# Kernel optimization log

Measured on AMD Instinct MI355X. Metric: run time of the kernel, lower is better.

## Reference

```python
import jax, jax.numpy as jnp
import numpy as np

N_NODES = 10000
N_EDGES = 640000
NF = 64    # node_feature_size
EF = 64    # edge_feature_size
NH = 128   # node_hidden_size
EH = 128   # edge_hidden_size
CS = 128   # context_size


def _linear_init(key, fan_in, shape):
    bound = 1.0 / np.sqrt(fan_in)
    return jax.random.uniform(key, shape, jnp.float32, -bound, bound)


def setup_inputs() -> dict:
    key = jax.random.key(0)
    ks = jax.random.split(key, 20)
    node_feats = jax.random.normal(ks[0], (N_NODES, NF), jnp.float32)
    edge_feats = jax.random.normal(ks[1], (N_EDGES, EF), jnp.float32)
    src = jax.random.randint(ks[2], (N_EDGES,), 0, N_NODES, jnp.int32)
    dst = jax.random.randint(ks[3], (N_EDGES,), 0, N_NODES, jnp.int32)
    return {
        "node_feats": node_feats,
        "edge_feats": edge_feats,
        "W_node": _linear_init(ks[4], NF, (NF, NH)),
        "b_node": _linear_init(ks[5], NF, (NH,)),
        "W_edge": _linear_init(ks[6], NF + EF, (NF + EF, EH)),
        "b_edge": _linear_init(ks[7], NF + EF, (EH,)),
        "W_logit": _linear_init(ks[8], NH + EH, (NH + EH, 1)),
        "b_logit": _linear_init(ks[9], NH + EH, (1,)),
        "W_msg": _linear_init(ks[10], EH, (EH, CS)),
        "b_msg": _linear_init(ks[11], EH, (CS,)),
        "W_ih": _linear_init(ks[12], NH, (3 * NH, CS)),   # torch GRUCell weight_ih layout
        "W_hh": _linear_init(ks[13], NH, (3 * NH, NH)),
        "b_ih": _linear_init(ks[14], NH, (3 * NH,)),
        "b_hh": _linear_init(ks[15], NH, (3 * NH,)),
        "src": src,
        "dst": dst,
    }


def reference(node_feats, edge_feats, W_node, b_node, W_edge, b_edge,
              W_logit, b_logit, W_msg, b_msg, W_ih, W_hh, b_ih, b_hh,
              src, dst):
    n_nodes = node_feats.shape[0]
    # (1) embed nodes: h_v = LeakyReLU(Linear(f_v))
    h_v = jax.nn.leaky_relu(node_feats @ W_node + b_node)          # [N, NH]
    # (2) embed edges from [src node feats, edge feats]
    e_in = jnp.concatenate([node_feats[src], edge_feats], axis=1)  # [M, NF+EF]
    h_e = jax.nn.leaky_relu(e_in @ W_edge + b_edge)                # [M, EH]
    # raw messages T(h_w->v)
    m = h_e @ W_msg + b_msg                                        # [M, CS]
    # (3) attention logits from [src node hidden, edge hidden]
    l_in = jnp.concatenate([h_v[src], h_e], axis=1)                # [M, NH+EH]
    logit = jax.nn.leaky_relu(l_in @ W_logit + b_logit)            # [M, 1]
    # (4) edge softmax grouped by destination node
    lmax = jax.ops.segment_max(logit, dst, num_segments=n_nodes)   # [N, 1]
    ex = jnp.exp(logit - lmax[dst])
    den = jax.ops.segment_sum(ex, dst, num_segments=n_nodes)       # [N, 1]
    alpha = ex / den[dst]                                          # [M, 1]
    # (5) weighted segment-sum context, then elu
    C_v = jax.ops.segment_sum(alpha * m, dst, num_segments=n_nodes)  # [N, CS]
    C_v = jax.nn.elu(C_v)
    # (6) GRUCell(input=C_v, hidden=h_v), torch semantics, then ReLU
    gi = C_v @ W_ih.T + b_ih                                       # [N, 3*NH]
    gh = h_v @ W_hh.T + b_hh
    i_r, i_z, i_n = jnp.split(gi, 3, axis=1)
    h_r, h_z, h_n = jnp.split(gh, 3, axis=1)
    r = jax.nn.sigmoid(i_r + h_r)
    z = jax.nn.sigmoid(i_z + h_z)
    n = jnp.tanh(i_n + r * h_n)
    h_new = jax.nn.relu((1.0 - z) * n + z * h_v)                   # [N, NH]
    # update_edges=False -> return original edge feats alongside new node states
    return h_new, edge_feats
```

## Files before the change

### kernel.cpp

```cpp
#include <hip/hip_runtime.h>
#include <hip/hip_bf16.h>

typedef unsigned short u16;
typedef unsigned int u32;

typedef __attribute__((ext_vector_type(8))) short bf16x8;
typedef __attribute__((ext_vector_type(4))) float f32x4;

__device__ __forceinline__ u16 f2bf(float f) {
    u32 u = __float_as_uint(f);
    u32 r = ((u >> 16) & 1u) + 0x7fffu;
    return (u16)((u + r) >> 16);
}
__device__ __forceinline__ float bf2f(u16 u) {
    return __uint_as_float(((u32)u) << 16);
}
__device__ __forceinline__ float leaky(float x) { return x >= 0.f ? x : 0.01f * x; }

__global__ __launch_bounds__(256) void k_prep_transpose(
    const float* __restrict__ We, u16* __restrict__ WeT)
{
    int idx = blockIdx.x * 256 + threadIdx.x;
    int r = (idx >> 7) & 127;
    int c = idx & 127;
    WeT[c * 128 + r] = f2bf(We[r * 128 + c]);
}

__global__ __launch_bounds__(256) void k_csr_count(
    const int* __restrict__ dst, u32* __restrict__ deg, int nE)
{
    long e = (long)blockIdx.x * 256 + threadIdx.x;
    if (e >= nE) return;
    atomicAdd(&deg[dst[e]], 1u);
}

__global__ __launch_bounds__(256) void k_csr_scan(
    const u32* __restrict__ deg, u32* __restrict__ start,
    u32* __restrict__ cur, int nN)
{
    __shared__ u32 s[256];
    int t = threadIdx.x;
    int chunk = (nN + 255) / 256;
    int a = t * chunk;
    int b = a + chunk; if (b > nN) b = nN; if (a > nN) a = nN;
    u32 sum = 0;
    for (int i = a; i < b; i++) sum += deg[i];
    s[t] = sum;
    __syncthreads();
    for (int d = 1; d < 256; d <<= 1) {
        u32 v = (t >= d) ? s[t - d] : 0u;
        __syncthreads();
        s[t] += v;
        __syncthreads();
    }
    u32 base = (t == 0) ? 0u : s[t - 1];
    for (int i = a; i < b; i++) { start[i] = base; cur[i] = base; base += deg[i]; }
}

__global__ __launch_bounds__(256) void k_csr_scatter(
    const int* __restrict__ src, const int* __restrict__ dst,
    u32* __restrict__ cur, int* __restrict__ sEidG,
    int* __restrict__ sSrcG, int* __restrict__ sDstG,
    int* __restrict__ rank, int nE)
{
    long e = (long)blockIdx.x * 256 + threadIdx.x;
    if (e >= nE) return;
    int d = dst[e];
    u32 p = atomicAdd(&cur[d], 1u);
    sEidG[p] = (int)e;
    sSrcG[p] = src[e];
    sDstG[p] = d;
    rank[e] = (int)p;
}

__global__ __launch_bounds__(128) void k_node_embed(
    const float* __restrict__ nf, const float* __restrict__ Wn,
    const float* __restrict__ bn, const float* __restrict__ WL,
    float* __restrict__ h_v, float* __restrict__ g, int nN)
{
    __shared__ float sW[64][128];
    __shared__ float sF[8][64];
    __shared__ float sRed[2][8];
    int j = threadIdx.x;
    int n0 = blockIdx.x * 8;
    for (int i = 0; i < 64; i++) sW[i][j] = Wn[i * 128 + j];
    for (int t = j; t < 8 * 64; t += 128) {
        int n = t >> 6, k = t & 63;
        int nn = n0 + n; if (nn >= nN) nn = nN - 1;
        sF[n][k] = nf[(long)nn * 64 + k];
    }
    __syncthreads();
    float bj = bn[j];
    float wl = WL[j];
    int wv = j >> 6, ln = j & 63;
    float hval[8];
    for (int n = 0; n < 8; n++) {
        float acc = bj;
        #pragma unroll 16
        for (int k = 0; k < 64; k++) acc += sF[n][k] * sW[k][j];
        float h = leaky(acc);
        hval[n] = h;
        if (n0 + n < nN) h_v[(long)(n0 + n) * 128 + j] = h;
    }
    #pragma unroll
    for (int n = 0; n < 8; n++) {
        float part = hval[n] * wl;
        #pragma unroll
        for (int o = 1; o < 64; o <<= 1) part += __shfl_xor(part, o);
        if (ln == 0) sRed[wv][n] = part;
    }
    __syncthreads();
    if (j < 8 && n0 + j < nN) g[n0 + j] = sRed[0][j] + sRed[1][j];
}

__device__ __forceinline__ void stage_ein(
    u16 (*sIn)[136], const float* nf, const float* ef,
    const int* sSrc, long e0, int nE, int tid)
{
    for (int c = tid; c < 64 * 32; c += 256) {
        int e = c >> 5, p = c & 31;
        long eg = e0 + e; if (eg >= nE) eg = nE - 1;
        float4 v;
        if (p < 16) v = *((const float4*)(nf + (long)sSrc[e] * 64 + p * 4));
        else        v = *((const float4*)(ef + eg * 64 + (p - 16) * 4));
        u32 lo = (u32)f2bf(v.x) | ((u32)f2bf(v.y) << 16);
        u32 hi = (u32)f2bf(v.z) | ((u32)f2bf(v.w) << 16);
        *((u32*)&sIn[e][p * 4])     = lo;
        *((u32*)&sIn[e][p * 4 + 2]) = hi;
    }
}

template<bool WRITE_HE>
__global__ __launch_bounds__(256) void k_edge_logit(
    const float* __restrict__ nf, const float* __restrict__ ef,
    const int* __restrict__ src, const int* __restrict__ rank,
    const u16* __restrict__ WeT, const float* __restrict__ be,
    const float* __restrict__ WL, const float* __restrict__ bL,
    const float* __restrict__ g,
    float* __restrict__ logitS, u16* __restrict__ heG, int nE)
{
    __shared__ u16 sW[128][136];
    __shared__ u16 sIn[64][136];
    __shared__ float sWL2[128];
    __shared__ int sSrc[64];
    __shared__ int sRank[64];
    int tid = threadIdx.x;
    long e0 = (long)blockIdx.x * 64;
    if (tid < 64) {
        long eg = e0 + tid; if (eg >= nE) eg = nE - 1;
        sSrc[tid] = src[eg];
        sRank[tid] = rank[eg];
    } else if (tid < 192) {
        sWL2[tid - 64] = WL[tid + 64];
    }
    __syncthreads();
    for (int c = tid; c < 2048; c += 256) {
        int r = c >> 4, p = c & 15;
        *((uint4*)&sW[r][p * 8]) = *((const uint4*)(WeT + r * 128 + p * 8));
    }
    stage_ein(sIn, nf, ef, sSrc, e0, nE, tid);
    __syncthreads();

    int lane = tid & 63, w = tid >> 6;
    int nl = lane & 15, q = lane >> 4;
    f32x4 acc[8];
    #pragma unroll
    for (int t = 0; t < 8; t++) acc[t] = (f32x4){0.f, 0.f, 0.f, 0.f};
    int eA = w * 16 + nl;
    #pragma unroll
    for (int s = 0; s < 4; s++) {
        int k0 = s * 32 + q * 8;
        bf16x8 a = *((const bf16x8*)&sIn[eA][k0]);
        #pragma unroll
        for (int t = 0; t < 8; t++) {
            bf16x8 b = *((const bf16x8*)&sW[t * 16 + nl][k0]);
            acc[t] = __builtin_amdgcn_mfma_f32_16x16x32_bf16(a, b, acc[t], 0, 0, 0);
        }
    }
    #pragma unroll
    for (int t = 0; t < 8; t++) {
        int col = t * 16 + nl;
        float bias = be[col];
        #pragma unroll
        for (int r = 0; r < 4; r++) {
            int e = w * 16 + q * 4 + r;
            sIn[e][col] = f2bf(leaky(acc[t][r] + bias));
        }
    }
    if (WRITE_HE) {
        #pragma unroll
        for (int i = 0; i < 4; i++) {
            int row = w * 16 + i * 4 + (lane >> 4);
            int ch = lane & 15;
            long eg = e0 + row;
            uint4 v4 = *((const uint4*)&sIn[row][ch * 8]);
            if (eg < nE) *((uint4*)(heG + eg * 128 + ch * 8)) = v4;
        }
    }
    int ew = lane >> 2, sub = lane & 3;
    int e = w * 16 + ew;
    float sum = 0.f;
    #pragma unroll
    for (int i = 0; i < 4; i++) {
        bf16x8 hv = *((const bf16x8*)&sIn[e][sub * 32 + i * 8]);
        #pragma unroll
        for (int jj = 0; jj < 8; jj++)
            sum += bf2f((u16)hv[jj]) * sWL2[sub * 32 + i * 8 + jj];
    }
    sum += __shfl_xor(sum, 1);
    sum += __shfl_xor(sum, 2);
    if (sub == 0 && e0 + e < nE) {
        float l = leaky(sum + g[sSrc[e]] + bL[0]);
        logitS[sRank[e]] = l;
    }
}

__global__ __launch_bounds__(256) void k_softmax_node(
    const u32* __restrict__ start, const u32* __restrict__ deg,
    float* __restrict__ logitS, int nN)
{
    int v = blockIdx.x * 4 + (threadIdx.x >> 6);
    int lane = threadIdx.x & 63;
    if (v >= nN) return;
    u32 d = deg[v];
    if (d == 0) return;
    u32 s0 = start[v];
    float mx = -3.402823e38f;
    for (u32 i = lane; i < d; i += 64) mx = fmaxf(mx, logitS[s0 + i]);
    #pragma unroll
    for (int o = 1; o < 64; o <<= 1) mx = fmaxf(mx, __shfl_xor(mx, o));
    float sum = 0.f;
    for (u32 i = lane; i < d; i += 64) {
        float e = __expf(logitS[s0 + i] - mx);
        logitS[s0 + i] = e;
        sum += e;
    }
    #pragma unroll
    for (int o = 1; o < 64; o <<= 1) sum += __shfl_xor(sum, o);
    float inv = 1.f / sum;
    for (u32 i = lane; i < d; i += 64) logitS[s0 + i] *= inv;
}

__global__ __launch_bounds__(256) void k_msg_lite(
    const u16* __restrict__ heG, const float* __restrict__ alphaS,
    const int* __restrict__ sEidG, const int* __restrict__ sDstG,
    float* __restrict__ A, int nE)
{
    __shared__ float sAl[256];
    __shared__ int sEid[256];
    __shared__ int sDst[256];
    int tid = threadIdx.x;
    long p0 = (long)blockIdx.x * 256;
    long p = p0 + tid;
    if (p < nE) {
        sAl[tid] = alphaS[p];
        sEid[tid] = sEidG[p];
        sDst[tid] = sDstG[p];
    } else {
        sAl[tid] = 0.f;
        sEid[tid] = sEidG[nE - 1];
        sDst[tid] = sDstG[nE - 1];
    }
    __syncthreads();
    int lane = tid & 63, w = tid >> 6;
    int i0 = w * 64;
    float sx = 0.f, sy = 0.f;
    int curd = sDst[i0];
    #pragma unroll 4
    for (int i = 0; i < 64; i++) {
        int idx = i0 + i;
        float a = sAl[idx];
        const u16* row = heG + (long)sEid[idx] * 128;
        sx += a * bf2f(row[lane]);
        sy += a * bf2f(row[lane + 64]);
        int nxt = (i == 63) ? -1 : sDst[idx + 1];
        if (nxt != curd) {
            atomicAdd(&A[(long)curd * 128 + lane], sx);
            atomicAdd(&A[(long)curd * 128 + lane + 64], sy);
            sx = 0.f; sy = 0.f;
            curd = nxt;
        }
    }
}

__global__ __launch_bounds__(256) void k_msg_heavy(
    const float* __restrict__ nf, const float* __restrict__ ef,
    const int* __restrict__ sEidG, const int* __restrict__ sSrcG,
    const int* __restrict__ sDstG,
    const u16* __restrict__ WeT, const float* __restrict__ be,
    const float* __restrict__ alphaS,
    float* __restrict__ A, int nE)
{
    __shared__ u16 sW[128][136];
    __shared__ u16 sIn[64][136];
    __shared__ float sAlpha[64];
    __shared__ int sSrc[64];
    __shared__ int sEid[64];
    __shared__ int sDst[64];
    int tid = threadIdx.x;
    long p0 = (long)blockIdx.x * 64;
    if (tid < 64) {
        long p = p0 + tid;
        if (p < nE) {
            sEid[tid] = sEidG[p];
            sSrc[tid] = sSrcG[p];
            sDst[tid] = sDstG[p];
            sAlpha[tid] = alphaS[p];
        } else {
            sEid[tid] = sEidG[nE - 1];
            sSrc[tid] = sSrcG[nE - 1];
            sDst[tid] = sDstG[nE - 1];
            sAlpha[tid] = 0.f;
        }
    }
    __syncthreads();
    for (int c = tid; c < 2048; c += 256) {
        int r = c >> 4, pp = c & 15;
        *((uint4*)&sW[r][pp * 8]) = *((const uint4*)(WeT + r * 128 + pp * 8));
    }
    for (int c = tid; c < 64 * 32; c += 256) {
        int e = c >> 5, pp = c & 31;
        float4 v;
        if (pp < 16) v = *((const float4*)(nf + (long)sSrc[e] * 64 + pp * 4));
        else         v = *((const float4*)(ef + (long)sEid[e] * 64 + (pp - 16) * 4));
        u32 lo = (u32)f2bf(v.x) | ((u32)f2bf(v.y) << 16);
        u32 hi = (u32)f2bf(v.z) | ((u32)f2bf(v.w) << 16);
        *((u32*)&sIn[e][pp * 4])     = lo;
        *((u32*)&sIn[e][pp * 4 + 2]) = hi;
    }
    __syncthreads();

    int lane = tid & 63, w = tid >> 6;
    int nl = lane & 15, q = lane >> 4;
    f32x4 acc[8];
    #pragma unroll
    for (int t = 0; t < 8; t++) acc[t] = (f32x4){0.f, 0.f, 0.f, 0.f};
    int eA = w * 16 + nl;
    #pragma unroll
    for (int s = 0; s < 4; s++) {
        int k0 = s * 32 + q * 8;
        bf16x8 a = *((const bf16x8*)&sIn[eA][k0]);
        #pragma unroll
        for (int t = 0; t < 8; t++) {
            bf16x8 b = *((const bf16x8*)&sW[t * 16 + nl][k0]);
            acc[t] = __builtin_amdgcn_mfma_f32_16x16x32_bf16(a, b, acc[t], 0, 0, 0);
        }
    }
    #pragma unroll
    for (int t = 0; t < 8; t++) {
        int col = t * 16 + nl;
        float bias = be[col];
        #pragma unroll
        for (int r = 0; r < 4; r++) {
            int e = w * 16 + q * 4 + r;
            sIn[e][col] = f2bf(leaky(acc[t][r] + bias));
        }
    }
    int eb = w * 16;
    float sx = 0.f, sy = 0.f;
    int curd = sDst[eb];
    for (int i = 0; i < 16; i++) {
        int e = eb + i;
        float a = sAlpha[e];
        sx += a * bf2f(sIn[e][lane]);
        sy += a * bf2f(sIn[e][lane + 64]);
        int nxt = (i == 15) ? -1 : sDst[e + 1];
        if (nxt != curd) {
            atomicAdd(&A[(long)curd * 128 + lane], sx);
            atomicAdd(&A[(long)curd * 128 + lane + 64], sy);
            sx = 0.f; sy = 0.f;
            curd = nxt;
        }
    }
}

__global__ __launch_bounds__(128) void k_gru(
    const float* __restrict__ h_v, const float* __restrict__ A,
    const float* __restrict__ Wm, const float* __restrict__ bm,
    const u32* __restrict__ deg,
    const float* __restrict__ Wih, const float* __restrict__ Whh,
    const float* __restrict__ bih, const float* __restrict__ bhh,
    float* __restrict__ out, int nN)
{
    __shared__ float sA[8][128];
    __shared__ float sC[8][128];
    __shared__ float sH[8][128];
    int j = threadIdx.x;
    int n0 = blockIdx.x * 8;
    for (int n = 0; n < 8; n++) {
        int nn = n0 + n; if (nn >= nN) nn = nN - 1;
        sA[n][j] = A[(long)nn * 128 + j];
        sH[n][j] = h_v[(long)nn * 128 + j];
    }
    __syncthreads();
    float cc[8];
    {
        float bmj = bm[j];
        #pragma unroll
        for (int n = 0; n < 8; n++) cc[n] = bmj;
        for (int k = 0; k < 128; k++) {
            float wk = Wm[(long)k * 128 + j];
            #pragma unroll
            for (int n = 0; n < 8; n++) cc[n] += sA[n][k] * wk;
        }
    }
    for (int n = 0; n < 8; n++) {
        int nn = n0 + n; if (nn >= nN) nn = nN - 1;
        float c = cc[n];
        sC[n][j] = (deg[nn] > 0u) ? (c > 0.f ? c : __expf(c) - 1.f) : 0.f;
    }
    __syncthreads();
    float gi[3][8], gh[3][8];
    #pragma unroll
    for (int g = 0; g < 3; g++) {
        float bi = bih[g * 128 + j];
        float bh = bhh[g * 128 + j];
        #pragma unroll
        for (int n = 0; n < 8; n++) { gi[g][n] = bi; gh[g][n] = bh; }
    }
    for (int k = 0; k < 128; k += 4) {
        float4 cv[8], hv[8];
        #pragma unroll
        for (int n = 0; n < 8; n++) {
            cv[n] = *(const float4*)&sC[n][k];
            hv[n] = *(const float4*)&sH[n][k];
        }
        #pragma unroll
        for (int g = 0; g < 3; g++) {
            float4 wi = *((const float4*)(Wih + (long)(g * 128 + j) * 128 + k));
            float4 wh = *((const float4*)(Whh + (long)(g * 128 + j) * 128 + k));
            #pragma unroll
            for (int n = 0; n < 8; n++) {
                gi[g][n] += wi.x * cv[n].x + wi.y * cv[n].y + wi.z * cv[n].z + wi.w * cv[n].w;
                gh[g][n] += wh.x * hv[n].x + wh.y * hv[n].y + wh.z * hv[n].z + wh.w * hv[n].w;
            }
        }
    }
    #pragma unroll
    for (int n = 0; n < 8; n++) {
        if (n0 + n >= nN) break;
        float r = 1.f / (1.f + __expf(-(gi[0][n] + gh[0][n])));
        float z = 1.f / (1.f + __expf(-(gi[1][n] + gh[1][n])));
        float nn = tanhf(gi[2][n] + r * gh[2][n]);
        float h = (1.f - z) * nn + z * sH[n][j];
        out[(long)(n0 + n) * 128 + j] = (h > 0.f ? h : 0.f);
    }
}

extern "C" void kernel_launch(void* const* d_in, const int* in_sizes, int n_in,
                              void* d_out, int out_size, void* d_ws, size_t ws_size,
                              hipStream_t stream) {
    const float* nf  = (const float*)d_in[0];
    const float* ef  = (const float*)d_in[1];
    const float* Wn  = (const float*)d_in[2];
    const float* bn  = (const float*)d_in[3];
    const float* We  = (const float*)d_in[4];
    const float* be  = (const float*)d_in[5];
    const float* WL  = (const float*)d_in[6];
    const float* bL  = (const float*)d_in[7];
    const float* Wm  = (const float*)d_in[8];
    const float* bm  = (const float*)d_in[9];
    const float* Wih = (const float*)d_in[10];
    const float* Whh = (const float*)d_in[11];
    const float* bih = (const float*)d_in[12];
    const float* bhh = (const float*)d_in[13];
    const int* src = (const int*)d_in[14];
    const int* dst = (const int*)d_in[15];
    float* out = (float*)d_out;

    int nN = in_sizes[0] / 64;
    int nE = in_sizes[1] / 64;

    size_t o = 0;
    auto nxt = [&](size_t b) { size_t p = o; o += (b + 255) & ~(size_t)255; return p; };
    size_t o_hv    = nxt((size_t)nN * 128 * 4);
    size_t o_g     = nxt((size_t)nN * 4);
    size_t o_logit = nxt((size_t)nE * 4);
    size_t o_A     = nxt((size_t)nN * 128 * 4);
    size_t o_deg   = nxt((size_t)nN * 4);
    size_t o_start = nxt((size_t)nN * 4);
    size_t o_cur   = nxt((size_t)nN * 4);
    size_t o_eid   = nxt((size_t)nE * 4);
    size_t o_srcS  = nxt((size_t)nE * 4);
    size_t o_dstS  = nxt((size_t)nE * 4);
    size_t o_rank  = nxt((size_t)nE * 4);
    size_t o_WeT   = nxt((size_t)128 * 128 * 2);
    size_t o_he    = nxt((size_t)nE * 128 * 2);
    bool lite = (o <= ws_size);

    char* w = (char*)d_ws;
    float* h_v    = (float*)(w + o_hv);
    float* g      = (float*)(w + o_g);
    float* logitS = (float*)(w + o_logit);
    float* A      = (float*)(w + o_A);
    u32*   deg    = (u32*)(w + o_deg);
    u32*   start  = (u32*)(w + o_start);
    u32*   cur    = (u32*)(w + o_cur);
    int*   sEid   = (int*)(w + o_eid);
    int*   sSrcS  = (int*)(w + o_srcS);
    int*   sDstS  = (int*)(w + o_dstS);
    int*   rank   = (int*)(w + o_rank);
    u16*   WeT    = (u16*)(w + o_WeT);
    u16*   heG    = (u16*)(w + o_he);

    hipMemsetAsync(A, 0, o_start - o_A, stream);

    int gN8   = (nN + 7) / 8;
    int gN4   = (nN + 3) / 4;
    int gE64  = (nE + 63) / 64;
    int gE256 = (nE + 255) / 256;

    k_prep_transpose<<<64, 256, 0, stream>>>(We, WeT);
    k_csr_count<<<gE256, 256, 0, stream>>>(dst, deg, nE);
    k_csr_scan<<<1, 256, 0, stream>>>(deg, start, cur, nN);
    k_csr_scatter<<<gE256, 256, 0, stream>>>(src, dst, cur, sEid, sSrcS, sDstS, rank, nE);
    k_node_embed<<<gN8, 128, 0, stream>>>(nf, Wn, bn, WL, h_v, g, nN);
    if (lite) {
        k_edge_logit<true><<<gE64, 256, 0, stream>>>(
            nf, ef, src, rank, WeT, be, WL, bL, g, logitS, heG, nE);
    } else {
        k_edge_logit<false><<<gE64, 256, 0, stream>>>(
            nf, ef, src, rank, WeT, be, WL, bL, g, logitS, heG, nE);
    }
    k_softmax_node<<<gN4, 256, 0, stream>>>(start, deg, logitS, nN);
    if (lite) {
        k_msg_lite<<<gE256, 256, 0, stream>>>(heG, logitS, sEid, sDstS, A, nE);
    } else {
        k_msg_heavy<<<gE64, 256, 0, stream>>>(nf, ef, sEid, sSrcS, sDstS,
                                              WeT, be, logitS, A, nE);
    }
    k_gru<<<gN8, 128, 0, stream>>>(h_v, A, Wm, bm, deg,
                                   Wih, Whh, bih, bhh, out, nN);

    hipMemcpyAsync(out + (size_t)nN * 128, ef, (size_t)nE * 64 * 4,
                   hipMemcpyDeviceToDevice, stream);
}
```

Before: 829.4 us.

## Process edges in dst-sorted order, fuse softmax with aggregation, drop atomics and memcpy

The edge-logit kernel now walks edges in CSR (destination-sorted) order, so logits and h_e rows land contiguously and the rank array goes away. Edge softmax and the weighted message sum are fused into one per-node wavefront kernel that accumulates h_e rows directly, with no atomics, and writes A once. The edge-feature passthrough copy is folded into the edge kernel's staging loads instead of a separate memcpy. The weight tile is split into two 64-row halves to cut LDS use and raise occupancy. The tradeoff is uncoalesced gathers of edge_feats by sorted eid, a serial per-node loop whose length follows degree, and a memset narrowed to deg only.

```diff
diff --git a/kernel.cpp b/kernel.cpp
--- a/kernel.cpp
+++ b/kernel.cpp
@@ -60,8 +60,7 @@
 __global__ __launch_bounds__(256) void k_csr_scatter(
     const int* __restrict__ src, const int* __restrict__ dst,
     u32* __restrict__ cur, int* __restrict__ sEidG,
-    int* __restrict__ sSrcG, int* __restrict__ sDstG,
-    int* __restrict__ rank, int nE)
+    int* __restrict__ sSrcG, int* __restrict__ sDstG, int nE)
 {
     long e = (long)blockIdx.x * 256 + threadIdx.x;
     if (e >= nE) return;
@@ -70,7 +69,6 @@
     sEidG[p] = (int)e;
     sSrcG[p] = src[e];
     sDstG[p] = d;
-    rank[e] = (int)p;
 }
 
 __global__ __launch_bounds__(128) void k_node_embed(
@@ -113,68 +111,88 @@
     if (j < 8 && n0 + j < nN) g[n0 + j] = sRed[0][j] + sRed[1][j];
 }
 
-__device__ __forceinline__ void stage_ein(
-    u16 (*sIn)[136], const float* nf, const float* ef,
-    const int* sSrc, long e0, int nE, int tid)
-{
-    for (int c = tid; c < 64 * 32; c += 256) {
+template<bool WRITE_HE>
+__global__ __launch_bounds__(256, 4) void k_edge_logit(
+    const float* __restrict__ nf, const float* __restrict__ ef,
+    const int* __restrict__ sEidG, const int* __restrict__ sSrcG,
+    const u16* __restrict__ WeT, const float* __restrict__ be,
+    const float* __restrict__ WL, const float* __restrict__ bL,
+    const float* __restrict__ g,
+    float* __restrict__ logitS, u16* __restrict__ heG,
+    float* __restrict__ efOut, int nE)
+{
+    __shared__ u16 sW[64][136];
+    __shared__ u16 sIn[64][136];
+    __shared__ float sWL2[128];
+    __shared__ float sG[64];
+    __shared__ int sSrc[64];
+    __shared__ int sEid[64];
+    int tid = threadIdx.x;
+    long p0 = (long)blockIdx.x * 64;
+    if (tid < 64) {
+        long p = p0 + tid; if (p >= nE) p = nE - 1;
+        int eid = sEidG[p];
+        int s = sSrcG[p];
+        sEid[tid] = eid;
+        sSrc[tid] = s;
+        sG[tid] = g[s];
+    } else if (tid < 192) {
+        sWL2[tid - 64] = WL[64 + tid];
+    }
+    __syncthreads();
+    for (int c = tid; c < 1024; c += 256) {
+        int r = c >> 4, p = c & 15;
+        *((uint4*)&sW[r][p * 8]) = *((const uint4*)(WeT + r * 128 + p * 8));
+    }
+    for (int c = tid; c < 2048; c += 256) {
         int e = c >> 5, p = c & 31;
-        long eg = e0 + e; if (eg >= nE) eg = nE - 1;
         float4 v;
-        if (p < 16) v = *((const float4*)(nf + (long)sSrc[e] * 64 + p * 4));
-        else        v = *((const float4*)(ef + eg * 64 + (p - 16) * 4));
+        if (p < 16) {
+            v = *((const float4*)(nf + (long)sSrc[e] * 64 + p * 4));
+        } else {
+            v = *((const float4*)(ef + (long)sEid[e] * 64 + (p - 16) * 4));
+            if (p0 + e < nE)
+                *((float4*)(efOut + (long)sEid[e] * 64 + (p - 16) * 4)) = v;
+        }
         u32 lo = (u32)f2bf(v.x) | ((u32)f2bf(v.y) << 16);
         u32 hi = (u32)f2bf(v.z) | ((u32)f2bf(v.w) << 16);
         *((u32*)&sIn[e][p * 4])     = lo;
         *((u32*)&sIn[e][p * 4 + 2]) = hi;
     }
-}
-
-template<bool WRITE_HE>
-__global__ __launch_bounds__(256) void k_edge_logit(
-    const float* __restrict__ nf, const float* __restrict__ ef,
-    const int* __restrict__ src, const int* __restrict__ rank,
-    const u16* __restrict__ WeT, const float* __restrict__ be,
-    const float* __restrict__ WL, const float* __restrict__ bL,
-    const float* __restrict__ g,
-    float* __restrict__ logitS, u16* __restrict__ heG, int nE)
-{
-    __shared__ u16 sW[128][136];
-    __shared__ u16 sIn[64][136];
-    __shared__ float sWL2[128];
-    __shared__ int sSrc[64];
-    __shared__ int sRank[64];
-    int tid = threadIdx.x;
-    long e0 = (long)blockIdx.x * 64;
-    if (tid < 64) {
-        long eg = e0 + tid; if (eg >= nE) eg = nE - 1;
-        sSrc[tid] = src[eg];
-        sRank[tid] = rank[eg];
-    } else if (tid < 192) {
-        sWL2[tid - 64] = WL[tid + 64];
-    }
-    __syncthreads();
-    for (int c = tid; c < 2048; c += 256) {
-        int r = c >> 4, p = c & 15;
-        *((uint4*)&sW[r][p * 8]) = *((const uint4*)(WeT + r * 128 + p * 8));
-    }
-    stage_ein(sIn, nf, ef, sSrc, e0, nE, tid);
     __syncthreads();
 
     int lane = tid & 63, w = tid >> 6;
     int nl = lane & 15, q = lane >> 4;
+    int eA = w * 16 + nl;
+    bf16x8 afr[4];
+    #pragma unroll
+    for (int s = 0; s < 4; s++)
+        afr[s] = *((const bf16x8*)&sIn[eA][s * 32 + q * 8]);
     f32x4 acc[8];
     #pragma unroll
     for (int t = 0; t < 8; t++) acc[t] = (f32x4){0.f, 0.f, 0.f, 0.f};
-    int eA = w * 16 + nl;
     #pragma unroll
     for (int s = 0; s < 4; s++) {
         int k0 = s * 32 + q * 8;
-        bf16x8 a = *((const bf16x8*)&sIn[eA][k0]);
-        #pragma unroll
-        for (int t = 0; t < 8; t++) {
+        #pragma unroll
+        for (int t = 0; t < 4; t++) {
             bf16x8 b = *((const bf16x8*)&sW[t * 16 + nl][k0]);
-            acc[t] = __builtin_amdgcn_mfma_f32_16x16x32_bf16(a, b, acc[t], 0, 0, 0);
+            acc[t] = __builtin_amdgcn_mfma_f32_16x16x32_bf16(afr[s], b, acc[t], 0, 0, 0);
+        }
+    }
+    __syncthreads();
+    for (int c = tid; c < 1024; c += 256) {
+        int r = c >> 4, p = c & 15;
+        *((uint4*)&sW[r][p * 8]) = *((const uint4*)(WeT + (64 + r) * 128 + p * 8));
+    }
+    __syncthreads();
+    #pragma unroll
+    for (int s = 0; s < 4; s++) {
+        int k0 = s * 32 + q * 8;
+        #pragma unroll
+        for (int t = 0; t < 4; t++) {
+            bf16x8 b = *((const bf16x8*)&sW[t * 16 + nl][k0]);
+            acc[4 + t] = __builtin_amdgcn_mfma_f32_16x16x32_bf16(afr[s], b, acc[4 + t], 0, 0, 0);
         }
     }
     #pragma unroll
@@ -192,9 +210,9 @@
         for (int i = 0; i < 4; i++) {
             int row = w * 16 + i * 4 + (lane >> 4);
             int ch = lane & 15;
-            long eg = e0 + row;
+            long pg = p0 + row;
             uint4 v4 = *((const uint4*)&sIn[row][ch * 8]);
-            if (eg < nE) *((uint4*)(heG + eg * 128 + ch * 8)) = v4;
+            if (pg < nE) *((uint4*)(heG + pg * 128 + ch * 8)) = v4;
         }
     }
     int ew = lane >> 2, sub = lane & 3;
@@ -209,10 +227,53 @@
     }
     sum += __shfl_xor(sum, 1);
     sum += __shfl_xor(sum, 2);
-    if (sub == 0 && e0 + e < nE) {
-        float l = leaky(sum + g[sSrc[e]] + bL[0]);
-        logitS[sRank[e]] = l;
-    }
+    if (sub == 0 && p0 + e < nE) {
+        float l = leaky(sum + sG[e] + bL[0]);
+        logitS[p0 + e] = l;
+    }
+}
+
+__global__ __launch_bounds__(256) void k_softmax_msg(
+    const u32* __restrict__ start, const u32* __restrict__ deg,
+    const u16* __restrict__ heG, float* __restrict__ logitS,
+    float* __restrict__ A, int nN)
+{
+    __shared__ float sAl[4][1024];
+    int wv = threadIdx.x >> 6, lane = threadIdx.x & 63;
+    int v = blockIdx.x * 4 + wv;
+    if (v >= nN) return;
+    long base = (long)v * 128;
+    u32 d = deg[v];
+    if (d == 0) {
+        A[base + lane] = 0.f;
+        A[base + lane + 64] = 0.f;
+        return;
+    }
+    u32 s0 = start[v];
+    float mx = -3.402823e38f;
+    for (u32 i = lane; i < d; i += 64) mx = fmaxf(mx, logitS[s0 + i]);
+    #pragma unroll
+    for (int o = 1; o < 64; o <<= 1) mx = fmaxf(mx, __shfl_xor(mx, o));
+    float sum = 0.f;
+    for (u32 i = lane; i < d; i += 64) {
+        float e_ = __expf(logitS[s0 + i] - mx);
+        sum += e_;
+        if (i < 1024) sAl[wv][i] = e_;
+        else logitS[s0 + i] = e_;
+    }
+    #pragma unroll
+    for (int o = 1; o < 64; o <<= 1) sum += __shfl_xor(sum, o);
+    float inv = 1.f / sum;
+    float ax = 0.f, ay = 0.f;
+    #pragma unroll 4
+    for (u32 i = 0; i < d; i++) {
+        float al = (i < 1024) ? sAl[wv][i] : logitS[s0 + i];
+        u32 rw = *((const u32*)(heG + ((long)(s0 + i)) * 128 + lane * 2));
+        ax += al * bf2f((u16)(rw & 0xffffu));
+        ay += al * bf2f((u16)(rw >> 16));
+    }
+    A[base + lane * 2]     = ax * inv;
+    A[base + lane * 2 + 1] = ay * inv;
 }
 
 __global__ __launch_bounds__(256) void k_softmax_node(
@@ -239,48 +300,6 @@
     for (int o = 1; o < 64; o <<= 1) sum += __shfl_xor(sum, o);
     float inv = 1.f / sum;
     for (u32 i = lane; i < d; i += 64) logitS[s0 + i] *= inv;
-}
-
-__global__ __launch_bounds__(256) void k_msg_lite(
-    const u16* __restrict__ heG, const float* __restrict__ alphaS,
-    const int* __restrict__ sEidG, const int* __restrict__ sDstG,
-    float* __restrict__ A, int nE)
-{
-    __shared__ float sAl[256];
-    __shared__ int sEid[256];
-    __shared__ int sDst[256];
-    int tid = threadIdx.x;
-    long p0 = (long)blockIdx.x * 256;
-    long p = p0 + tid;
-    if (p < nE) {
-        sAl[tid] = alphaS[p];
-        sEid[tid] = sEidG[p];
-        sDst[tid] = sDstG[p];
-    } else {
-        sAl[tid] = 0.f;
-        sEid[tid] = sEidG[nE - 1];
-        sDst[tid] = sDstG[nE - 1];
-    }
-    __syncthreads();
-    int lane = tid & 63, w = tid >> 6;
-    int i0 = w * 64;
-    float sx = 0.f, sy = 0.f;
-    int curd = sDst[i0];
-    #pragma unroll 4
-    for (int i = 0; i < 64; i++) {
-        int idx = i0 + i;
-        float a = sAl[idx];
-        const u16* row = heG + (long)sEid[idx] * 128;
-        sx += a * bf2f(row[lane]);
-        sy += a * bf2f(row[lane + 64]);
-        int nxt = (i == 63) ? -1 : sDst[idx + 1];
-        if (nxt != curd) {
-            atomicAdd(&A[(long)curd * 128 + lane], sx);
-            atomicAdd(&A[(long)curd * 128 + lane + 64], sy);
-            sx = 0.f; sy = 0.f;
-            curd = nxt;
-        }
-    }
 }
 
 __global__ __launch_bounds__(256) void k_msg_heavy(
@@ -483,7 +502,6 @@
     size_t o_eid   = nxt((size_t)nE * 4);
     size_t o_srcS  = nxt((size_t)nE * 4);
     size_t o_dstS  = nxt((size_t)nE * 4);
-    size_t o_rank  = nxt((size_t)nE * 4);
     size_t o_WeT   = nxt((size_t)128 * 128 * 2);
     size_t o_he    = nxt((size_t)nE * 128 * 2);
     bool lite = (o <= ws_size);
@@ -499,11 +517,15 @@
     int*   sEid   = (int*)(w + o_eid);
     int*   sSrcS  = (int*)(w + o_srcS);
     int*   sDstS  = (int*)(w + o_dstS);
-    int*   rank   = (int*)(w + o_rank);
     u16*   WeT    = (u16*)(w + o_WeT);
     u16*   heG    = (u16*)(w + o_he);
-
-    hipMemsetAsync(A, 0, o_start - o_A, stream);
+    float* efOut  = out + (size_t)nN * 128;
+
+    if (lite) {
+        hipMemsetAsync(deg, 0, (size_t)nN * 4, stream);
+    } else {
+        hipMemsetAsync(A, 0, o_start - o_A, stream);
+    }
 
     int gN8   = (nN + 7) / 8;
     int gN4   = (nN + 3) / 4;
@@ -513,25 +535,19 @@
     k_prep_transpose<<<64, 256, 0, stream>>>(We, WeT);
     k_csr_count<<<gE256, 256, 0, stream>>>(dst, deg, nE);
     k_csr_scan<<<1, 256, 0, stream>>>(deg, start, cur, nN);
-    k_csr_scatter<<<gE256, 256, 0, stream>>>(src, dst, cur, sEid, sSrcS, sDstS, rank, nE);
+    k_csr_scatter<<<gE256, 256, 0, stream>>>(src, dst, cur, sEid, sSrcS, sDstS, nE);
     k_node_embed<<<gN8, 128, 0, stream>>>(nf, Wn, bn, WL, h_v, g, nN);
     if (lite) {
         k_edge_logit<true><<<gE64, 256, 0, stream>>>(
-            nf, ef, src, rank, WeT, be, WL, bL, g, logitS, heG, nE);
+            nf, ef, sEid, sSrcS, WeT, be, WL, bL, g, logitS, heG, efOut, nE);
+        k_softmax_msg<<<gN4, 256, 0, stream>>>(start, deg, heG, logitS, A, nN);
     } else {
         k_edge_logit<false><<<gE64, 256, 0, stream>>>(
-            nf, ef, src, rank, WeT, be, WL, bL, g, logitS, heG, nE);
-    }
-    k_softmax_node<<<gN4, 256, 0, stream>>>(start, deg, logitS, nN);
-    if (lite) {
-        k_msg_lite<<<gE256, 256, 0, stream>>>(heG, logitS, sEid, sDstS, A, nE);
-    } else {
+            nf, ef, sEid, sSrcS, WeT, be, WL, bL, g, logitS, heG, efOut, nE);
+        k_softmax_node<<<gN4, 256, 0, stream>>>(start, deg, logitS, nN);
         k_msg_heavy<<<gE64, 256, 0, stream>>>(nf, ef, sEid, sSrcS, sDstS,
                                               WeT, be, logitS, A, nE);
     }
     k_gru<<<gN8, 128, 0, stream>>>(h_v, A, Wm, bm, deg,
                                    Wih, Whh, bih, bhh, out, nN);
-
-    hipMemcpyAsync(out + (size_t)nN * 128, ef, (size_t)nE * 64 * 4,
-                   hipMemcpyDeviceToDevice, stream);
-}
+}
```

Result: faster. 746.8 us (-10.0%).
